# Performance work log

Hardware: AMD Instinct MI355X
Metric: run time of the kernel (lower is better)

## Reference

```python
import jax, jax.numpy as jnp
import numpy as np

ITERATIONS = 20
EPS = 1e-9

def setup_inputs() -> dict:
    key = jax.random.key(0)
    x = jax.random.normal(key, (8192, 64, 64), dtype=jnp.float32)
    return {"x": x}

def reference(x):
    M = jnp.exp(x)
    def body(_, M):
        M = M / (jnp.sum(M, axis=-1, keepdims=True) + EPS)
        M = M / (jnp.sum(M, axis=-2, keepdims=True) + EPS)
        return M
    M = jax.lax.fori_loop(0, ITERATIONS, body, M)
    return M
```

## Files before the change

kernel.cpp:

```cpp
#include <hip/hip_runtime.h>

#define ITERS 20
#define EPS 1e-9f


template <int CTRL>
__device__ __forceinline__ float dpp_add(float x) {
    int yi = __builtin_amdgcn_update_dpp(0, __float_as_int(x), CTRL, 0xf, 0xf, true);
    return x + __int_as_float(yi);
}

__global__ __launch_bounds__(256, 4) void sinkhorn_kernel(
        const float* __restrict__ x, float* __restrict__ out, int nmat) {
    const int lane = threadIdx.x & 63;
    const int wave = threadIdx.x >> 6;
    const int mat  = blockIdx.x * 4 + wave;
    if (mat >= nmat) return;
    const int bi = lane >> 3;
    const int bj = lane & 7;

    const float4* __restrict__ xin = (const float4*)(x + (size_t)mat * 4096);

    float b[8][8];
    #pragma unroll
    for (int r = 0; r < 8; ++r) {
        float4 lo = xin[(8 * bi + r) * 16 + 2 * bj + 0];
        float4 hi = xin[(8 * bi + r) * 16 + 2 * bj + 1];
        b[r][0] = __expf(lo.x); b[r][1] = __expf(lo.y);
        b[r][2] = __expf(lo.z); b[r][3] = __expf(lo.w);
        b[r][4] = __expf(hi.x); b[r][5] = __expf(hi.y);
        b[r][6] = __expf(hi.z); b[r][7] = __expf(hi.w);
    }

    float uu[8], vv[8];
    #pragma unroll
    for (int i = 0; i < 8; ++i) { uu[i] = 1.0f; vv[i] = 1.0f; }

    for (int it = 0; it < ITERS; ++it) {
        float p[8];
        #pragma unroll
        for (int r = 0; r < 8; ++r) {
            float s = 0.0f;
            #pragma unroll
            for (int c = 0; c < 8; ++c) s = fmaf(b[r][c], vv[c], s);
            p[r] = s;
        }
        #pragma unroll
        for (int r = 0; r < 8; ++r) p[r] = dpp_add<0xB1>(p[r]);
        #pragma unroll
        for (int r = 0; r < 8; ++r) p[r] = dpp_add<0x4E>(p[r]);
        #pragma unroll
        for (int r = 0; r < 8; ++r) p[r] = dpp_add<0x141>(p[r]);
        #pragma unroll
        for (int r = 0; r < 8; ++r) {
            float S = fmaf(uu[r], p[r], EPS);
            uu[r] *= __builtin_amdgcn_rcpf(S);
        }

        float q[8];
        #pragma unroll
        for (int c = 0; c < 8; ++c) {
            float s = 0.0f;
            #pragma unroll
            for (int r = 0; r < 8; ++r) s = fmaf(b[r][c], uu[r], s);
            q[c] = s;
        }
        #pragma unroll
        for (int c = 0; c < 8; ++c) q[c] = dpp_add<0x128>(q[c]);
        #pragma unroll
        for (int c = 0; c < 8; ++c) q[c] += __shfl_xor(q[c], 16, 64);
        #pragma unroll
        for (int c = 0; c < 8; ++c) q[c] += __shfl_xor(q[c], 32, 64);
        #pragma unroll
        for (int c = 0; c < 8; ++c) {
            float T = fmaf(vv[c], q[c], EPS);
            vv[c] *= __builtin_amdgcn_rcpf(T);
        }
    }

    float4* __restrict__ o = (float4*)(out + (size_t)mat * 4096);
    #pragma unroll
    for (int r = 0; r < 8; ++r) {
        float ur = uu[r];
        float4 lo, hi;
        lo.x = b[r][0] * ur * vv[0]; lo.y = b[r][1] * ur * vv[1];
        lo.z = b[r][2] * ur * vv[2]; lo.w = b[r][3] * ur * vv[3];
        hi.x = b[r][4] * ur * vv[4]; hi.y = b[r][5] * ur * vv[5];
        hi.z = b[r][6] * ur * vv[6]; hi.w = b[r][7] * ur * vv[7];
        o[(8 * bi + r) * 16 + 2 * bj + 0] = lo;
        o[(8 * bi + r) * 16 + 2 * bj + 1] = hi;
    }
}

extern "C" void kernel_launch(void* const* d_in, const int* in_sizes, int n_in,
                              void* d_out, int out_size, void* d_ws, size_t ws_size,
                              hipStream_t stream) {
    const float* x = (const float*)d_in[0];
    float* out = (float*)d_out;
    const int nmat = in_sizes[0] / 4096;
    const int blocks = (nmat + 3) / 4;
    sinkhorn_kernel<<<blocks, 256, 0, stream>>>(x, out, nmat);
}
```

Before: 250.6 us.

## Use packed float2 math and permlane swaps for Sinkhorn scaling reductions

```diff
diff --git a/kernel.cpp b/kernel.cpp
--- a/kernel.cpp
+++ b/kernel.cpp
@@ -2,6 +2,8 @@
 
 #define ITERS 20
 #define EPS 1e-9f
+
+typedef float v2f __attribute__((ext_vector_type(2)));
 
 
 template <int CTRL>
@@ -9,6 +11,30 @@
     int yi = __builtin_amdgcn_update_dpp(0, __float_as_int(x), CTRL, 0xf, 0xf, true);
     return x + __int_as_float(yi);
 }
+
+#if __has_builtin(__builtin_amdgcn_permlane16_swap)
+__device__ __forceinline__ float xadd16(float x) {
+    unsigned u = __float_as_uint(x);
+    auto r = __builtin_amdgcn_permlane16_swap(u, u, false, false);
+    return __uint_as_float(r[0]) + __uint_as_float(r[1]);
+}
+#else
+__device__ __forceinline__ float xadd16(float x) {
+    return x + __int_as_float(__builtin_amdgcn_ds_swizzle(__float_as_int(x), 0x401F));
+}
+#endif
+
+#if __has_builtin(__builtin_amdgcn_permlane32_swap)
+__device__ __forceinline__ float xadd32(float x) {
+    unsigned u = __float_as_uint(x);
+    auto r = __builtin_amdgcn_permlane32_swap(u, u, false, false);
+    return __uint_as_float(r[0]) + __uint_as_float(r[1]);
+}
+#else
+__device__ __forceinline__ float xadd32(float x) {
+    return x + __shfl_xor(x, 32, 64);
+}
+#endif
 
 __global__ __launch_bounds__(256, 4) void sinkhorn_kernel(
         const float* __restrict__ x, float* __restrict__ out, int nmat) {
@@ -21,29 +47,33 @@
 
     const float4* __restrict__ xin = (const float4*)(x + (size_t)mat * 4096);
 
-    float b[8][8];
+    v2f b2[8][4];
     #pragma unroll
     for (int r = 0; r < 8; ++r) {
         float4 lo = xin[(8 * bi + r) * 16 + 2 * bj + 0];
         float4 hi = xin[(8 * bi + r) * 16 + 2 * bj + 1];
-        b[r][0] = __expf(lo.x); b[r][1] = __expf(lo.y);
-        b[r][2] = __expf(lo.z); b[r][3] = __expf(lo.w);
-        b[r][4] = __expf(hi.x); b[r][5] = __expf(hi.y);
-        b[r][6] = __expf(hi.z); b[r][7] = __expf(hi.w);
+        b2[r][0] = (v2f){__expf(lo.x), __expf(lo.y)};
+        b2[r][1] = (v2f){__expf(lo.z), __expf(lo.w)};
+        b2[r][2] = (v2f){__expf(hi.x), __expf(hi.y)};
+        b2[r][3] = (v2f){__expf(hi.z), __expf(hi.w)};
     }
 
-    float uu[8], vv[8];
+    float uu[8];
+    v2f   vv2[4];
     #pragma unroll
-    for (int i = 0; i < 8; ++i) { uu[i] = 1.0f; vv[i] = 1.0f; }
+    for (int i = 0; i < 8; ++i) uu[i] = 1.0f;
+    #pragma unroll
+    for (int i = 0; i < 4; ++i) vv2[i] = (v2f){1.0f, 1.0f};
 
     for (int it = 0; it < ITERS; ++it) {
         float p[8];
         #pragma unroll
         for (int r = 0; r < 8; ++r) {
-            float s = 0.0f;
-            #pragma unroll
-            for (int c = 0; c < 8; ++c) s = fmaf(b[r][c], vv[c], s);
-            p[r] = s;
+            v2f s2 = b2[r][0] * vv2[0];
+            s2 += b2[r][1] * vv2[1];
+            s2 += b2[r][2] * vv2[2];
+            s2 += b2[r][3] * vv2[3];
+            p[r] = s2.x + s2.y;
         }
         #pragma unroll
         for (int r = 0; r < 8; ++r) p[r] = dpp_add<0xB1>(p[r]);
@@ -57,36 +87,52 @@
             uu[r] *= __builtin_amdgcn_rcpf(S);
         }
 
-        float q[8];
+        v2f q2[4];
         #pragma unroll
-        for (int c = 0; c < 8; ++c) {
-            float s = 0.0f;
+        for (int c = 0; c < 4; ++c) q2[c] = b2[0][c] * uu[0];
+        #pragma unroll
+        for (int r = 1; r < 8; ++r) {
             #pragma unroll
-            for (int r = 0; r < 8; ++r) s = fmaf(b[r][c], uu[r], s);
-            q[c] = s;
+            for (int c = 0; c < 4; ++c) q2[c] += b2[r][c] * uu[r];
         }
         #pragma unroll
-        for (int c = 0; c < 8; ++c) q[c] = dpp_add<0x128>(q[c]);
+        for (int c = 0; c < 4; ++c) {
+            q2[c].x = dpp_add<0x128>(q2[c].x);
+            q2[c].y = dpp_add<0x128>(q2[c].y);
+        }
         #pragma unroll
-        for (int c = 0; c < 8; ++c) q[c] += __shfl_xor(q[c], 16, 64);
+        for (int c = 0; c < 4; ++c) {
+            q2[c].x = xadd16(q2[c].x);
+            q2[c].y = xadd16(q2[c].y);
+        }
         #pragma unroll
-        for (int c = 0; c < 8; ++c) q[c] += __shfl_xor(q[c], 32, 64);
+        for (int c = 0; c < 4; ++c) {
+            q2[c].x = xadd32(q2[c].x);
+            q2[c].y = xadd32(q2[c].y);
+        }
         #pragma unroll
-        for (int c = 0; c < 8; ++c) {
-            float T = fmaf(vv[c], q[c], EPS);
-            vv[c] *= __builtin_amdgcn_rcpf(T);
+        for (int c = 0; c < 4; ++c) {
+            float Tx = fmaf(vv2[c].x, q2[c].x, EPS);
+            float Ty = fmaf(vv2[c].y, q2[c].y, EPS);
+            vv2[c].x *= __builtin_amdgcn_rcpf(Tx);
+            vv2[c].y *= __builtin_amdgcn_rcpf(Ty);
         }
     }
 
     float4* __restrict__ o = (float4*)(out + (size_t)mat * 4096);
     #pragma unroll
     for (int r = 0; r < 8; ++r) {
-        float ur = uu[r];
+        v2f uv0 = vv2[0] * uu[r];
+        v2f uv1 = vv2[1] * uu[r];
+        v2f uv2 = vv2[2] * uu[r];
+        v2f uv3 = vv2[3] * uu[r];
+        v2f w0 = b2[r][0] * uv0;
+        v2f w1 = b2[r][1] * uv1;
+        v2f w2 = b2[r][2] * uv2;
+        v2f w3 = b2[r][3] * uv3;
         float4 lo, hi;
-        lo.x = b[r][0] * ur * vv[0]; lo.y = b[r][1] * ur * vv[1];
-        lo.z = b[r][2] * ur * vv[2]; lo.w = b[r][3] * ur * vv[3];
-        hi.x = b[r][4] * ur * vv[4]; hi.y = b[r][5] * ur * vv[5];
-        hi.z = b[r][6] * ur * vv[6]; hi.w = b[r][7] * ur * vv[7];
+        lo.x = w0.x; lo.y = w0.y; lo.z = w1.x; lo.w = w1.y;
+        hi.x = w2.x; hi.y = w2.y; hi.z = w3.x; hi.w = w3.y;
         o[(8 * bi + r) * 16 + 2 * bj + 0] = lo;
         o[(8 * bi + r) * 16 + 2 * bj + 1] = hi;
     }
```

New measurement: 250.1 us. About the same (-0.2%).

## Store exp matrix in fp16 and use dot2/fma_mix with permlane swaps

Applied to the files above, without the earlier changes.

```diff
diff --git a/kernel.cpp b/kernel.cpp
--- a/kernel.cpp
+++ b/kernel.cpp
@@ -2,12 +2,61 @@
 
 #define ITERS 20
 #define EPS 1e-9f
+
+typedef _Float16 v2h __attribute__((ext_vector_type(2)));
 
 
 template <int CTRL>
 __device__ __forceinline__ float dpp_add(float x) {
     int yi = __builtin_amdgcn_update_dpp(0, __float_as_int(x), CTRL, 0xf, 0xf, true);
     return x + __int_as_float(yi);
+}
+
+#if __has_builtin(__builtin_amdgcn_permlane16_swap)
+__device__ __forceinline__ float xadd16(float x) {
+    unsigned u = __float_as_uint(x);
+    auto r = __builtin_amdgcn_permlane16_swap(u, u, false, false);
+    return __uint_as_float(r[0]) + __uint_as_float(r[1]);
+}
+#else
+__device__ __forceinline__ float xadd16(float x) {
+    return x + __int_as_float(__builtin_amdgcn_ds_swizzle(__float_as_int(x), 0x401F));
+}
+#endif
+
+#if __has_builtin(__builtin_amdgcn_permlane32_swap)
+__device__ __forceinline__ float xadd32(float x) {
+    unsigned u = __float_as_uint(x);
+    auto r = __builtin_amdgcn_permlane32_swap(u, u, false, false);
+    return __uint_as_float(r[0]) + __uint_as_float(r[1]);
+}
+#else
+__device__ __forceinline__ float xadd32(float x) {
+    return x + __shfl_xor(x, 32, 64);
+}
+#endif
+
+__device__ __forceinline__ float dot2(v2h a, v2h b, float c) {
+#if __has_builtin(__builtin_amdgcn_fdot2)
+    return __builtin_amdgcn_fdot2(a, b, c, false);
+#else
+    float d;
+    asm("v_dot2_f32_f16 %0, %1, %2, %3" : "=v"(d) : "v"(a), "v"(b), "v"(c));
+    return d;
+#endif
+}
+
+__device__ __forceinline__ float fma_mix_lo(v2h a, float b, float c) {
+    float d;
+    asm("v_fma_mix_f32 %0, %1, %2, %3 op_sel:[0,0,0] op_sel_hi:[1,0,0]"
+        : "=v"(d) : "v"(a), "v"(b), "v"(c));
+    return d;
+}
+__device__ __forceinline__ float fma_mix_hi(v2h a, float b, float c) {
+    float d;
+    asm("v_fma_mix_f32 %0, %1, %2, %3 op_sel:[1,0,0] op_sel_hi:[1,0,0]"
+        : "=v"(d) : "v"(a), "v"(b), "v"(c));
+    return d;
 }
 
 __global__ __launch_bounds__(256, 4) void sinkhorn_kernel(
@@ -21,28 +70,32 @@
 
     const float4* __restrict__ xin = (const float4*)(x + (size_t)mat * 4096);
 
-    float b[8][8];
+    v2h eh[8][4];
     #pragma unroll
     for (int r = 0; r < 8; ++r) {
         float4 lo = xin[(8 * bi + r) * 16 + 2 * bj + 0];
         float4 hi = xin[(8 * bi + r) * 16 + 2 * bj + 1];
-        b[r][0] = __expf(lo.x); b[r][1] = __expf(lo.y);
-        b[r][2] = __expf(lo.z); b[r][3] = __expf(lo.w);
-        b[r][4] = __expf(hi.x); b[r][5] = __expf(hi.y);
-        b[r][6] = __expf(hi.z); b[r][7] = __expf(hi.w);
+        eh[r][0] = (v2h){(_Float16)__expf(lo.x), (_Float16)__expf(lo.y)};
+        eh[r][1] = (v2h){(_Float16)__expf(lo.z), (_Float16)__expf(lo.w)};
+        eh[r][2] = (v2h){(_Float16)__expf(hi.x), (_Float16)__expf(hi.y)};
+        eh[r][3] = (v2h){(_Float16)__expf(hi.z), (_Float16)__expf(hi.w)};
     }
 
     float uu[8], vv[8];
+    v2h vh[4];
     #pragma unroll
     for (int i = 0; i < 8; ++i) { uu[i] = 1.0f; vv[i] = 1.0f; }
+    #pragma unroll
+    for (int i = 0; i < 4; ++i) vh[i] = (v2h){(_Float16)1.0f, (_Float16)1.0f};
 
     for (int it = 0; it < ITERS; ++it) {
         float p[8];
         #pragma unroll
         for (int r = 0; r < 8; ++r) {
-            float s = 0.0f;
-            #pragma unroll
-            for (int c = 0; c < 8; ++c) s = fmaf(b[r][c], vv[c], s);
+            float s = dot2(eh[r][0], vh[0], 0.0f);
+            s = dot2(eh[r][1], vh[1], s);
+            s = dot2(eh[r][2], vh[2], s);
+            s = dot2(eh[r][3], vh[3], s);
             p[r] = s;
         }
         #pragma unroll
@@ -52,41 +105,52 @@
         #pragma unroll
         for (int r = 0; r < 8; ++r) p[r] = dpp_add<0x141>(p[r]);
         #pragma unroll
-        for (int r = 0; r < 8; ++r) {
-            float S = fmaf(uu[r], p[r], EPS);
-            uu[r] *= __builtin_amdgcn_rcpf(S);
-        }
+        for (int r = 0; r < 8; ++r)
+            uu[r] = __builtin_amdgcn_rcpf(p[r] + EPS);
 
         float q[8];
         #pragma unroll
-        for (int c = 0; c < 8; ++c) {
-            float s = 0.0f;
+        for (int c2 = 0; c2 < 4; ++c2) {
+            q[2 * c2 + 0] = fma_mix_lo(eh[0][c2], uu[0], 0.0f);
+            q[2 * c2 + 1] = fma_mix_hi(eh[0][c2], uu[0], 0.0f);
+        }
+        #pragma unroll
+        for (int r = 1; r < 8; ++r) {
             #pragma unroll
-            for (int r = 0; r < 8; ++r) s = fmaf(b[r][c], uu[r], s);
-            q[c] = s;
+            for (int c2 = 0; c2 < 4; ++c2) {
+                q[2 * c2 + 0] = fma_mix_lo(eh[r][c2], uu[r], q[2 * c2 + 0]);
+                q[2 * c2 + 1] = fma_mix_hi(eh[r][c2], uu[r], q[2 * c2 + 1]);
+            }
         }
         #pragma unroll
         for (int c = 0; c < 8; ++c) q[c] = dpp_add<0x128>(q[c]);
         #pragma unroll
-        for (int c = 0; c < 8; ++c) q[c] += __shfl_xor(q[c], 16, 64);
+        for (int c = 0; c < 8; ++c) q[c] = xadd16(q[c]);
         #pragma unroll
-        for (int c = 0; c < 8; ++c) q[c] += __shfl_xor(q[c], 32, 64);
+        for (int c = 0; c < 8; ++c) q[c] = xadd32(q[c]);
         #pragma unroll
-        for (int c = 0; c < 8; ++c) {
-            float T = fmaf(vv[c], q[c], EPS);
-            vv[c] *= __builtin_amdgcn_rcpf(T);
-        }
+        for (int c = 0; c < 8; ++c)
+            vv[c] = __builtin_amdgcn_rcpf(q[c] + EPS);
+        #pragma unroll
+        for (int c2 = 0; c2 < 4; ++c2)
+            vh[c2] = (v2h){(_Float16)vv[2 * c2], (_Float16)vv[2 * c2 + 1]};
     }
 
     float4* __restrict__ o = (float4*)(out + (size_t)mat * 4096);
     #pragma unroll
     for (int r = 0; r < 8; ++r) {
         float ur = uu[r];
+        float uv0 = ur * vv[0], uv1 = ur * vv[1], uv2 = ur * vv[2], uv3 = ur * vv[3];
+        float uv4 = ur * vv[4], uv5 = ur * vv[5], uv6 = ur * vv[6], uv7 = ur * vv[7];
         float4 lo, hi;
-        lo.x = b[r][0] * ur * vv[0]; lo.y = b[r][1] * ur * vv[1];
-        lo.z = b[r][2] * ur * vv[2]; lo.w = b[r][3] * ur * vv[3];
-        hi.x = b[r][4] * ur * vv[4]; hi.y = b[r][5] * ur * vv[5];
-        hi.z = b[r][6] * ur * vv[6]; hi.w = b[r][7] * ur * vv[7];
+        lo.x = fma_mix_lo(eh[r][0], uv0, 0.0f);
+        lo.y = fma_mix_hi(eh[r][0], uv1, 0.0f);
+        lo.z = fma_mix_lo(eh[r][1], uv2, 0.0f);
+        lo.w = fma_mix_hi(eh[r][1], uv3, 0.0f);
+        hi.x = fma_mix_lo(eh[r][2], uv4, 0.0f);
+        hi.y = fma_mix_hi(eh[r][2], uv5, 0.0f);
+        hi.z = fma_mix_lo(eh[r][3], uv6, 0.0f);
+        hi.w = fma_mix_hi(eh[r][3], uv7, 0.0f);
         o[(8 * bi + r) * 16 + 2 * bj + 0] = lo;
         o[(8 * bi + r) * 16 + 2 * bj + 1] = hi;
     }
```

New measurement: 256.0 us. +2.2%, slower.

## Process several matrices per wave with double-buffered prefetch and cheaper cross-lane reductions

Applied to the files above, without the earlier changes.

```diff
diff --git a/kernel.cpp b/kernel.cpp
--- a/kernel.cpp
+++ b/kernel.cpp
@@ -2,6 +2,7 @@
 
 #define ITERS 20
 #define EPS 1e-9f
+#define MPW 4
 
 
 template <int CTRL>
@@ -10,29 +11,52 @@
     return x + __int_as_float(yi);
 }
 
-__global__ __launch_bounds__(256, 4) void sinkhorn_kernel(
-        const float* __restrict__ x, float* __restrict__ out, int nmat) {
-    const int lane = threadIdx.x & 63;
-    const int wave = threadIdx.x >> 6;
-    const int mat  = blockIdx.x * 4 + wave;
-    if (mat >= nmat) return;
-    const int bi = lane >> 3;
-    const int bj = lane & 7;
+#if __has_builtin(__builtin_amdgcn_permlane16_swap)
+__device__ __forceinline__ float xadd16(float x) {
+    unsigned u = __float_as_uint(x);
+    auto r = __builtin_amdgcn_permlane16_swap(u, u, false, false);
+    return __uint_as_float(r[0]) + __uint_as_float(r[1]);
+}
+#else
+__device__ __forceinline__ float xadd16(float x) {
+    return x + __int_as_float(__builtin_amdgcn_ds_swizzle(__float_as_int(x), 0x401F));
+}
+#endif
 
+#if __has_builtin(__builtin_amdgcn_permlane32_swap)
+__device__ __forceinline__ float xadd32(float x) {
+    unsigned u = __float_as_uint(x);
+    auto r = __builtin_amdgcn_permlane32_swap(u, u, false, false);
+    return __uint_as_float(r[0]) + __uint_as_float(r[1]);
+}
+#else
+__device__ __forceinline__ float xadd32(float x) {
+    return x + __shfl_xor(x, 32, 64);
+}
+#endif
+
+__device__ __forceinline__ void load_raw(float (&d)[8][8], const float* __restrict__ x,
+                                         int mat, int bi, int bj) {
     const float4* __restrict__ xin = (const float4*)(x + (size_t)mat * 4096);
-
-    float b[8][8];
     #pragma unroll
     for (int r = 0; r < 8; ++r) {
         float4 lo = xin[(8 * bi + r) * 16 + 2 * bj + 0];
         float4 hi = xin[(8 * bi + r) * 16 + 2 * bj + 1];
-        b[r][0] = __expf(lo.x); b[r][1] = __expf(lo.y);
-        b[r][2] = __expf(lo.z); b[r][3] = __expf(lo.w);
-        b[r][4] = __expf(hi.x); b[r][5] = __expf(hi.y);
-        b[r][6] = __expf(hi.z); b[r][7] = __expf(hi.w);
+        d[r][0] = lo.x; d[r][1] = lo.y; d[r][2] = lo.z; d[r][3] = lo.w;
+        d[r][4] = hi.x; d[r][5] = hi.y; d[r][6] = hi.z; d[r][7] = hi.w;
     }
+}
 
-    float uu[8], vv[8];
+__device__ __forceinline__ void exp_inplace(float (&d)[8][8]) {
+    #pragma unroll
+    for (int r = 0; r < 8; ++r)
+        #pragma unroll
+        for (int c = 0; c < 8; ++c)
+            d[r][c] = __expf(d[r][c]);
+}
+
+__device__ __forceinline__ void sink_iters(const float (&b)[8][8],
+                                           float (&uu)[8], float (&vv)[8]) {
     #pragma unroll
     for (int i = 0; i < 8; ++i) { uu[i] = 1.0f; vv[i] = 1.0f; }
 
@@ -40,10 +64,15 @@
         float p[8];
         #pragma unroll
         for (int r = 0; r < 8; ++r) {
-            float s = 0.0f;
-            #pragma unroll
-            for (int c = 0; c < 8; ++c) s = fmaf(b[r][c], vv[c], s);
-            p[r] = s;
+            float se = b[r][0] * vv[0];
+            float so = b[r][1] * vv[1];
+            se = fmaf(b[r][2], vv[2], se);
+            so = fmaf(b[r][3], vv[3], so);
+            se = fmaf(b[r][4], vv[4], se);
+            so = fmaf(b[r][5], vv[5], so);
+            se = fmaf(b[r][6], vv[6], se);
+            so = fmaf(b[r][7], vv[7], so);
+            p[r] = se + so;
         }
         #pragma unroll
         for (int r = 0; r < 8; ++r) p[r] = dpp_add<0xB1>(p[r]);
@@ -52,32 +81,38 @@
         #pragma unroll
         for (int r = 0; r < 8; ++r) p[r] = dpp_add<0x141>(p[r]);
         #pragma unroll
-        for (int r = 0; r < 8; ++r) {
-            float S = fmaf(uu[r], p[r], EPS);
-            uu[r] *= __builtin_amdgcn_rcpf(S);
-        }
+        for (int r = 0; r < 8; ++r)
+            uu[r] = __builtin_amdgcn_rcpf(p[r] + EPS);
 
         float q[8];
         #pragma unroll
         for (int c = 0; c < 8; ++c) {
-            float s = 0.0f;
-            #pragma unroll
-            for (int r = 0; r < 8; ++r) s = fmaf(b[r][c], uu[r], s);
-            q[c] = s;
+            float se = b[0][c] * uu[0];
+            float so = b[1][c] * uu[1];
+            se = fmaf(b[2][c], uu[2], se);
+            so = fmaf(b[3][c], uu[3], so);
+            se = fmaf(b[4][c], uu[4], se);
+            so = fmaf(b[5][c], uu[5], so);
+            se = fmaf(b[6][c], uu[6], se);
+            so = fmaf(b[7][c], uu[7], so);
+            q[c] = se + so;
         }
         #pragma unroll
         for (int c = 0; c < 8; ++c) q[c] = dpp_add<0x128>(q[c]);
         #pragma unroll
-        for (int c = 0; c < 8; ++c) q[c] += __shfl_xor(q[c], 16, 64);
+        for (int c = 0; c < 8; ++c) q[c] = xadd16(q[c]);
         #pragma unroll
-        for (int c = 0; c < 8; ++c) q[c] += __shfl_xor(q[c], 32, 64);
+        for (int c = 0; c < 8; ++c) q[c] = xadd32(q[c]);
         #pragma unroll
-        for (int c = 0; c < 8; ++c) {
-            float T = fmaf(vv[c], q[c], EPS);
-            vv[c] *= __builtin_amdgcn_rcpf(T);
-        }
+        for (int c = 0; c < 8; ++c)
+            vv[c] = __builtin_amdgcn_rcpf(q[c] + EPS);
     }
+}
 
+__device__ __forceinline__ void store_out(const float (&b)[8][8],
+                                          const float (&uu)[8], const float (&vv)[8],
+                                          float* __restrict__ out, int mat,
+                                          int bi, int bj) {
     float4* __restrict__ o = (float4*)(out + (size_t)mat * 4096);
     #pragma unroll
     for (int r = 0; r < 8; ++r) {
@@ -92,12 +127,40 @@
     }
 }
 
+__global__ __launch_bounds__(256, 2) void sinkhorn_kernel(
+        const float* __restrict__ x, float* __restrict__ out, int nmat) {
+    const int lane = threadIdx.x & 63;
+    const int wave = threadIdx.x >> 6;
+    const int wid  = blockIdx.x * 4 + wave;
+    const int mat0 = wid * MPW;
+    if (mat0 >= nmat) return;
+    const int bi = lane >> 3;
+    const int bj = lane & 7;
+
+    float A[8][8], B[8][8];
+    load_raw(A, x, mat0, bi, bj);
+
+    #pragma unroll
+    for (int m = 0; m < MPW; ++m) {
+        const int mat = mat0 + m;
+        if (mat >= nmat) break;
+        float (&cur)[8][8] = (m & 1) ? B : A;
+        float (&nxt)[8][8] = (m & 1) ? A : B;
+        if (m + 1 < MPW && mat + 1 < nmat)
+            load_raw(nxt, x, mat + 1, bi, bj);
+        exp_inplace(cur);
+        float uu[8], vv[8];
+        sink_iters(cur, uu, vv);
+        store_out(cur, uu, vv, out, mat, bi, bj);
+    }
+}
+
 extern "C" void kernel_launch(void* const* d_in, const int* in_sizes, int n_in,
                               void* d_out, int out_size, void* d_ws, size_t ws_size,
                               hipStream_t stream) {
     const float* x = (const float*)d_in[0];
     float* out = (float*)d_out;
     const int nmat = in_sizes[0] / 4096;
-    const int blocks = (nmat + 3) / 4;
+    const int blocks = (nmat + 4 * MPW - 1) / (4 * MPW);
     sinkhorn_kernel<<<blocks, 256, 0, stream>>>(x, out, nmat);
 }
```

New measurement: 268.5 us. 1.07x slower.
